# Performance work log

Hardware: AMD Instinct MI355X
Metric: run time of the kernel (lower is better)

The kernel has to match this reference:

```python
import jax, jax.numpy as jnp
import numpy as np

D_MODEL = 512
N_STATE = 512  # must equal D_MODEL (torch code broadcasts B*(N,) against u[:,t] of (batch,d_model))
BATCH = 8
SEQ_LEN = 4096
DT_MIN, DT_MAX = 0.001, 0.1


def setup_inputs() -> dict:
    key = jax.random.key(0)
    k_u, k_lam, k_b, k_q, k_dt = jax.random.split(key, 5)
    u = jax.random.normal(k_u, (BATCH, SEQ_LEN, D_MODEL), dtype=jnp.float32)
    Lambda = jax.random.normal(k_lam, (N_STATE,), dtype=jnp.float32)
    B = jax.random.normal(k_b, (N_STATE,), dtype=jnp.float32)
    Q = jax.random.normal(k_q, (N_STATE, D_MODEL), dtype=jnp.float32) / np.sqrt(N_STATE)
    log_dt = jax.random.uniform(k_dt, (1,), dtype=jnp.float32) * (np.log(DT_MAX) - np.log(DT_MIN)) + np.log(DT_MIN)
    return {"u": u, "Lambda": Lambda, "B": B, "Q": Q, "log_dt": log_dt}


def reference(u, Lambda, B, Q, log_dt):
    # dt = exp(log_dt); A = diag(exp(dt * -exp(Lambda))) -> x @ A.T == x * a
    dt = jnp.exp(log_dt)              # (1,)
    a = jnp.exp(dt * (-jnp.exp(Lambda)))  # (N,)
    Bdt = dt * B                      # (N,)

    u_t = jnp.transpose(u, (1, 0, 2))  # (L, batch, N)

    def step(x, ut):
        x = x * a + Bdt * ut           # diagonal recurrence, (batch, N)
        return x, x

    x0 = jnp.zeros((u.shape[0], Lambda.shape[0]), dtype=u.dtype)
    _, xs = jax.lax.scan(step, x0, u_t)       # (L, batch, N)
    y = jnp.einsum('lbn,nd->bld', xs, Q)      # project to d_model
    return y
```

## Files before the change

### kernel.cpp

```cpp
#include <hip/hip_runtime.h>
#include <hip/hip_bf16.h>

#define BATCH 8
#define SEQ   4096
#define NST   512
#define DM    512
#define NCHUNK 64
#define TCH    64
#define NSUB   4
#define RSUB   16
#define LDP    (NST + 8)

typedef __attribute__((ext_vector_type(4))) float f32x4;
typedef __attribute__((ext_vector_type(8))) short short8v;
typedef __attribute__((ext_vector_type(4))) short short4v;

__device__ __forceinline__ short f2bf(float f) {
  union { float f; unsigned u; } v; v.f = f;
  unsigned r = v.u + 0x7FFFu + ((v.u >> 16) & 1u);
  return (short)(r >> 16);
}

__global__ void k_scan_sums(const float* __restrict__ u, const float* __restrict__ Lam,
                            const float* __restrict__ Bv, const float* __restrict__ log_dt,
                            float* __restrict__ S) {
  int gid = blockIdx.x * 128 + threadIdx.x;
  int n0 = (gid & 127) * 4;
  int bc = gid >> 7;
  int b  = bc & (BATCH - 1);
  int c  = bc >> 3;
  float dt = expf(log_dt[0]);
  f32x4 lam = *(const f32x4*)(Lam + n0);
  f32x4 bv  = *(const f32x4*)(Bv + n0);
  float a[4], g[4];
  #pragma unroll
  for (int i = 0; i < 4; ++i) { a[i] = expf(-dt * expf(lam[i])); g[i] = dt * bv[i]; }
  const float* up = u + ((size_t)b * SEQ + (size_t)c * TCH) * NST + n0;
  f32x4 s = (f32x4){0.f, 0.f, 0.f, 0.f};
  #pragma unroll 8
  for (int t = 0; t < TCH; ++t) {
    f32x4 v = *(const f32x4*)(up + (size_t)t * NST);
    #pragma unroll
    for (int i = 0; i < 4; ++i) s[i] = fmaf(a[i], s[i], g[i] * v[i]);
  }
  *(f32x4*)(S + (c * BATCH + b) * NST + n0) = s;
}

__global__ void k_propagate(const float* __restrict__ Lam, const float* __restrict__ log_dt,
                            const float* __restrict__ S, float* __restrict__ Xc) {
  int gid = blockIdx.x * 256 + threadIdx.x;
  int n = gid & (NST - 1);
  int b = gid >> 9;
  float dt = expf(log_dt[0]);
  float a  = expf(-dt * expf(Lam[n]));
  float aT = a;
  #pragma unroll
  for (int i = 0; i < 6; ++i) aT *= aT;
  float x = 0.f;
  for (int c = 0; c < NCHUNK; ++c) {
    Xc[(c * BATCH + b) * NST + n] = x;
    x = fmaf(aT, x, S[(c * BATCH + b) * NST + n]);
  }
}

__global__ void k_transQ(const float* __restrict__ Q, short* __restrict__ Qt) {
  __shared__ short tile[64][68];
  int bn = (blockIdx.x & 7) * 64;
  int bd = (blockIdx.x >> 3) * 64;
  int tc = threadIdx.x & 15;
  int tr = threadIdx.x >> 4;
  #pragma unroll
  for (int i = 0; i < 4; ++i) {
    int r = tr + i * 16;
    f32x4 v = *(const f32x4*)(Q + (size_t)(bn + r) * DM + bd + tc * 4);
    short4v h;
    h[0] = f2bf(v[0]); h[1] = f2bf(v[1]); h[2] = f2bf(v[2]); h[3] = f2bf(v[3]);
    *(short4v*)&tile[r][tc * 4] = h;
  }
  __syncthreads();
  #pragma unroll
  for (int i = 0; i < 4; ++i) {
    int r = tr + i * 16;
    short4v h;
    #pragma unroll
    for (int j = 0; j < 4; ++j) h[j] = tile[tc * 4 + j][r];
    *(short4v*)(Qt + (size_t)(bd + r) * NST + bn + tc * 4) = h;
  }
}

__global__ __launch_bounds__(512) void k_fused(
    const float* __restrict__ u, const float* __restrict__ Lam,
    const float* __restrict__ Bv, const float* __restrict__ log_dt,
    const float* __restrict__ Xc, const short* __restrict__ Qt,
    float* __restrict__ y) {
  __shared__ __align__(16) short X[TCH][LDP];
  __shared__ __align__(16) float Ssub[NSUB][NST];
  const int tid = threadIdx.x;
  const int b = blockIdx.x & (BATCH - 1);
  const int c = blockIdx.x >> 3;
  const int tq = tid >> 7;
  const int q  = tid & 127;
  const int n0 = q * 4;

  {
    const float dt = expf(log_dt[0]);
    f32x4 lam = *(const f32x4*)(Lam + n0);
    f32x4 bv  = *(const f32x4*)(Bv + n0);
    float a[4], g[4], a16[4];
    #pragma unroll
    for (int i = 0; i < 4; ++i) {
      a[i] = expf(-dt * expf(lam[i]));
      g[i] = dt * bv[i];
      float t = a[i]; t *= t; t *= t; t *= t; t *= t;
      a16[i] = t;
    }
    f32x4 seed = (f32x4){0.f, 0.f, 0.f, 0.f};
    if (tq == 0) seed = *(const f32x4*)(Xc + (c * BATCH + b) * NST + n0);

    const float* up = u + ((size_t)b * SEQ + (size_t)(c * TCH + tq * RSUB)) * NST + n0;
    f32x4 v[RSUB];
    #pragma unroll
    for (int j = 0; j < RSUB; ++j) v[j] = *(const f32x4*)(up + (size_t)j * NST);

    f32x4 x = seed;
    #pragma unroll
    for (int j = 0; j < RSUB; ++j) {
      #pragma unroll
      for (int i = 0; i < 4; ++i) x[i] = fmaf(a[i], x[i], g[i] * v[j][i]);
      v[j] = x;
    }
    *(f32x4*)&Ssub[tq][n0] = x;
    __syncthreads();

    if (tq > 0) {
      f32x4 I = *(const f32x4*)&Ssub[0][n0];
      for (int s = 1; s < tq; ++s) {
        f32x4 sv = *(const f32x4*)&Ssub[s][n0];
        #pragma unroll
        for (int i = 0; i < 4; ++i) I[i] = fmaf(a16[i], I[i], sv[i]);
      }
      f32x4 ap;
      #pragma unroll
      for (int i = 0; i < 4; ++i) ap[i] = a[i];
      #pragma unroll
      for (int j = 0; j < RSUB; ++j) {
        #pragma unroll
        for (int i = 0; i < 4; ++i) {
          v[j][i] = fmaf(ap[i], I[i], v[j][i]);
          ap[i] *= a[i];
        }
      }
    }
    #pragma unroll
    for (int j = 0; j < RSUB; ++j) {
      short4v h;
      h[0] = f2bf(v[j][0]); h[1] = f2bf(v[j][1]);
      h[2] = f2bf(v[j][2]); h[3] = f2bf(v[j][3]);
      *(short4v*)&X[tq * RSUB + j][n0] = h;
    }
  }
  __syncthreads();

  const int lane = tid & 63;
  const int wc   = tid >> 6;
  const int l15  = lane & 15;
  const int lhi  = lane >> 4;
  const int ka   = lhi * 8;
  const short* qbase = Qt + (size_t)(wc * 64 + l15) * NST + ka;
  float* yb = y + ((size_t)b * SEQ + (size_t)c * TCH) * DM;

  f32x4 acc[4][4];
  #pragma unroll
  for (int mi = 0; mi < 4; ++mi)
    #pragma unroll
    for (int nf = 0; nf < 4; ++nf) acc[mi][nf] = (f32x4){0.f, 0.f, 0.f, 0.f};

  #pragma unroll 4
  for (int kk = 0; kk < 16; ++kk) {
    const int k0 = kk * 32;
    short8v afrag[4];
    #pragma unroll
    for (int mi = 0; mi < 4; ++mi)
      afrag[mi] = *(const short8v*)&X[mi * 16 + l15][k0 + ka];
    short8v bfrag[4];
    #pragma unroll
    for (int nf = 0; nf < 4; ++nf)
      bfrag[nf] = *(const short8v*)(qbase + (size_t)nf * 16 * NST + k0);
    #pragma unroll
    for (int mi = 0; mi < 4; ++mi)
      #pragma unroll
      for (int nf = 0; nf < 4; ++nf)
        acc[mi][nf] = __builtin_amdgcn_mfma_f32_16x16x32_bf16(afrag[mi], bfrag[nf], acc[mi][nf], 0, 0, 0);
  }

  #pragma unroll
  for (int mi = 0; mi < 4; ++mi)
    #pragma unroll
    for (int nf = 0; nf < 4; ++nf) {
      const int rr = mi * 16 + lhi * 4;
      const int cc = wc * 64 + nf * 16 + l15;
      #pragma unroll
      for (int i = 0; i < 4; ++i)
        yb[(size_t)(rr + i) * DM + cc] = acc[mi][nf][i];
    }
}

extern "C" void kernel_launch(void* const* d_in, const int* in_sizes, int n_in,
                              void* d_out, int out_size, void* d_ws, size_t ws_size,
                              hipStream_t stream) {
  const float* u      = (const float*)d_in[0];
  const float* Lam    = (const float*)d_in[1];
  const float* Bv     = (const float*)d_in[2];
  const float* Q      = (const float*)d_in[3];
  const float* log_dt = (const float*)d_in[4];
  float* out = (float*)d_out;

  float* S  = (float*)d_ws;
  float* Xc = S + NCHUNK * BATCH * NST;
  short* Qt = (short*)(Xc + NCHUNK * BATCH * NST);

  hipLaunchKernelGGL(k_transQ, dim3(64), dim3(256), 0, stream, Q, Qt);
  hipLaunchKernelGGL(k_scan_sums, dim3(NCHUNK * BATCH), dim3(128), 0, stream,
                     u, Lam, Bv, log_dt, S);
  hipLaunchKernelGGL(k_propagate, dim3(BATCH * NST / 256), dim3(256), 0, stream,
                     Lam, log_dt, S, Xc);
  hipLaunchKernelGGL(k_fused, dim3(NCHUNK * BATCH), dim3(512), 0, stream,
                     u, Lam, Bv, log_dt, Xc, Qt, out);
}
```

Measured before the change: 70.79 us.

## Fuse scan pipeline into single cooperative kernel with grid sync

Replaces the four-kernel sequence (Q transpose, chunk sums, propagation, fused scan+GEMM) with one cooperative kernel. Each block computes its chunk-local scan once, keeps the u values in registers, publishes the chunk sum, grid-syncs, then directly reduces preceding chunk sums to get its carry-in before the MFMA projection. This removes launch overhead and the second read of u, at the cost of a grid-wide barrier and an O(c) redundant prefix reduction per block. If the cooperative launch fails, it falls back to the old path. The Qt transpose in the first 64 blocks is not ordered by a grid barrier before other blocks read Qt after the sync; it is written before the sync, so it is covered.

```diff
diff --git a/kernel.cpp b/kernel.cpp
--- a/kernel.cpp
+++ b/kernel.cpp
@@ -1,5 +1,8 @@
 #include <hip/hip_runtime.h>
 #include <hip/hip_bf16.h>
+#include <hip/hip_cooperative_groups.h>
+
+namespace cg = cooperative_groups;
 
 #define BATCH 8
 #define SEQ   4096
@@ -19,6 +22,180 @@
   union { float f; unsigned u; } v; v.f = f;
   unsigned r = v.u + 0x7FFFu + ((v.u >> 16) & 1u);
   return (short)(r >> 16);
+}
+
+__global__ __launch_bounds__(512) void k_mega(
+    const float* __restrict__ u, const float* __restrict__ Lam,
+    const float* __restrict__ Bv, const float* __restrict__ log_dt,
+    const float* __restrict__ Q, float* __restrict__ S,
+    short* __restrict__ Qt, float* __restrict__ y) {
+  __shared__ __align__(16) short X[TCH][LDP];
+  __shared__ __align__(16) float Ssub[NSUB][NST];
+  const int tid = threadIdx.x;
+  const int b = blockIdx.x & (BATCH - 1);
+  const int c = blockIdx.x >> 3;
+  const int tq = tid >> 7;
+  const int q  = tid & 127;
+  const int n0 = q * 4;
+
+  if (blockIdx.x < 64) {
+    short (*tile)[68] = (short(*)[68])&X[0][0];
+    const int bn = (blockIdx.x & 7) * 64;
+    const int bd = (blockIdx.x >> 3) * 64;
+    const int tc4 = (tid & 15) * 4;
+    const int tr = tid >> 4;
+    #pragma unroll
+    for (int i = 0; i < 2; ++i) {
+      int r = tr + i * 32;
+      f32x4 v = *(const f32x4*)(Q + (size_t)(bn + r) * DM + bd + tc4);
+      short4v h;
+      h[0] = f2bf(v[0]); h[1] = f2bf(v[1]); h[2] = f2bf(v[2]); h[3] = f2bf(v[3]);
+      *(short4v*)&tile[r][tc4] = h;
+    }
+    __syncthreads();
+    #pragma unroll
+    for (int i = 0; i < 2; ++i) {
+      int r = tr + i * 32;
+      short4v h;
+      #pragma unroll
+      for (int j = 0; j < 4; ++j) h[j] = tile[tc4 + j][r];
+      *(short4v*)(Qt + (size_t)(bd + r) * NST + bn + tc4) = h;
+    }
+    __syncthreads();
+  }
+
+  const float dtv = expf(log_dt[0]);
+  f32x4 lam = *(const f32x4*)(Lam + n0);
+  f32x4 bv  = *(const f32x4*)(Bv + n0);
+  float a[4], g[4], a16[4];
+  #pragma unroll
+  for (int i = 0; i < 4; ++i) {
+    a[i] = expf(-dtv * expf(lam[i]));
+    g[i] = dtv * bv[i];
+    float t = a[i]; t *= t; t *= t; t *= t; t *= t;
+    a16[i] = t;
+  }
+
+  const float* up = u + ((size_t)b * SEQ + (size_t)(c * TCH + tq * RSUB)) * NST + n0;
+  f32x4 v[RSUB];
+  #pragma unroll
+  for (int j = 0; j < RSUB; ++j) v[j] = *(const f32x4*)(up + (size_t)j * NST);
+  {
+    f32x4 x = (f32x4){0.f, 0.f, 0.f, 0.f};
+    #pragma unroll
+    for (int j = 0; j < RSUB; ++j) {
+      #pragma unroll
+      for (int i = 0; i < 4; ++i) x[i] = fmaf(a[i], x[i], g[i] * v[j][i]);
+      v[j] = x;
+    }
+    *(f32x4*)&Ssub[tq][n0] = x;
+  }
+  __syncthreads();
+
+  if (tq == 0) {
+    f32x4 s0 = *(const f32x4*)&Ssub[0][n0];
+    f32x4 s1 = *(const f32x4*)&Ssub[1][n0];
+    f32x4 s2 = *(const f32x4*)&Ssub[2][n0];
+    f32x4 s3 = *(const f32x4*)&Ssub[3][n0];
+    f32x4 cs;
+    #pragma unroll
+    for (int i = 0; i < 4; ++i)
+      cs[i] = fmaf(a16[i], fmaf(a16[i], fmaf(a16[i], s0[i], s1[i]), s2[i]), s3[i]);
+    *(f32x4*)(S + (c * BATCH + b) * NST + n0) = cs;
+  }
+  __threadfence();
+  cg::this_grid().sync();
+
+  float a64[4];
+  #pragma unroll
+  for (int i = 0; i < 4; ++i) { float t = a16[i]; t *= t; t *= t; a64[i] = t; }
+  f32x4 xin = (f32x4){0.f, 0.f, 0.f, 0.f};
+  {
+    int cp = 0;
+    for (; cp + 8 <= c; cp += 8) {
+      f32x4 sb[8];
+      #pragma unroll
+      for (int j = 0; j < 8; ++j) sb[j] = *(const f32x4*)(S + ((cp + j) * BATCH + b) * NST + n0);
+      #pragma unroll
+      for (int j = 0; j < 8; ++j)
+        #pragma unroll
+        for (int i = 0; i < 4; ++i) xin[i] = fmaf(a64[i], xin[i], sb[j][i]);
+    }
+    for (; cp < c; ++cp) {
+      f32x4 sv = *(const f32x4*)(S + (cp * BATCH + b) * NST + n0);
+      #pragma unroll
+      for (int i = 0; i < 4; ++i) xin[i] = fmaf(a64[i], xin[i], sv[i]);
+    }
+  }
+
+  f32x4 I = xin;
+  for (int s = 0; s < tq; ++s) {
+    f32x4 sv = *(const f32x4*)&Ssub[s][n0];
+    #pragma unroll
+    for (int i = 0; i < 4; ++i) I[i] = fmaf(a16[i], I[i], sv[i]);
+  }
+
+  {
+    f32x4 ap;
+    #pragma unroll
+    for (int i = 0; i < 4; ++i) ap[i] = a[i];
+    #pragma unroll
+    for (int j = 0; j < RSUB; ++j) {
+      short4v h;
+      #pragma unroll
+      for (int i = 0; i < 4; ++i) {
+        v[j][i] = fmaf(ap[i], I[i], v[j][i]);
+        ap[i] *= a[i];
+      }
+      h[0] = f2bf(v[j][0]); h[1] = f2bf(v[j][1]);
+      h[2] = f2bf(v[j][2]); h[3] = f2bf(v[j][3]);
+      *(short4v*)&X[tq * RSUB + j][n0] = h;
+    }
+  }
+  __syncthreads();
+
+  const int lane = tid & 63;
+  const int wc   = tid >> 6;
+  const int l15  = lane & 15;
+  const int lhi  = lane >> 4;
+  const int ka   = lhi * 8;
+  const short* qbase = Qt + (size_t)(wc * 64 + l15) * NST + ka;
+  float* yb = y + ((size_t)b * SEQ + (size_t)c * TCH) * DM;
+
+  f32x4 acc[4][4];
+  #pragma unroll
+  for (int mi = 0; mi < 4; ++mi)
+    #pragma unroll
+    for (int nf = 0; nf < 4; ++nf) acc[mi][nf] = (f32x4){0.f, 0.f, 0.f, 0.f};
+
+  #pragma unroll 4
+  for (int kk = 0; kk < 16; ++kk) {
+    const int k0 = kk * 32;
+    short8v afrag[4];
+    #pragma unroll
+    for (int mi = 0; mi < 4; ++mi)
+      afrag[mi] = *(const short8v*)&X[mi * 16 + l15][k0 + ka];
+    short8v bfrag[4];
+    #pragma unroll
+    for (int nf = 0; nf < 4; ++nf)
+      bfrag[nf] = *(const short8v*)(qbase + (size_t)nf * 16 * NST + k0);
+    #pragma unroll
+    for (int mi = 0; mi < 4; ++mi)
+      #pragma unroll
+      for (int nf = 0; nf < 4; ++nf)
+        acc[mi][nf] = __builtin_amdgcn_mfma_f32_16x16x32_bf16(afrag[mi], bfrag[nf], acc[mi][nf], 0, 0, 0);
+  }
+
+  #pragma unroll
+  for (int mi = 0; mi < 4; ++mi)
+    #pragma unroll
+    for (int nf = 0; nf < 4; ++nf) {
+      const int rr = mi * 16 + lhi * 4;
+      const int cc = wc * 64 + nf * 16 + l15;
+      #pragma unroll
+      for (int i = 0; i < 4; ++i)
+        yb[(size_t)(rr + i) * DM + cc] = acc[mi][nf][i];
+    }
 }
 
 __global__ void k_scan_sums(const float* __restrict__ u, const float* __restrict__ Lam,
@@ -101,7 +278,6 @@
   const int tq = tid >> 7;
   const int q  = tid & 127;
   const int n0 = q * 4;
-
   {
     const float dt = expf(log_dt[0]);
     f32x4 lam = *(const f32x4*)(Lam + n0);
@@ -116,12 +292,10 @@
     }
     f32x4 seed = (f32x4){0.f, 0.f, 0.f, 0.f};
     if (tq == 0) seed = *(const f32x4*)(Xc + (c * BATCH + b) * NST + n0);
-
     const float* up = u + ((size_t)b * SEQ + (size_t)(c * TCH + tq * RSUB)) * NST + n0;
     f32x4 v[RSUB];
     #pragma unroll
     for (int j = 0; j < RSUB; ++j) v[j] = *(const f32x4*)(up + (size_t)j * NST);
-
     f32x4 x = seed;
     #pragma unroll
     for (int j = 0; j < RSUB; ++j) {
@@ -131,7 +305,6 @@
     }
     *(f32x4*)&Ssub[tq][n0] = x;
     __syncthreads();
-
     if (tq > 0) {
       f32x4 I = *(const f32x4*)&Ssub[0][n0];
       for (int s = 1; s < tq; ++s) {
@@ -143,13 +316,12 @@
       #pragma unroll
       for (int i = 0; i < 4; ++i) ap[i] = a[i];
       #pragma unroll
-      for (int j = 0; j < RSUB; ++j) {
+      for (int j = 0; j < RSUB; ++j)
         #pragma unroll
         for (int i = 0; i < 4; ++i) {
           v[j][i] = fmaf(ap[i], I[i], v[j][i]);
           ap[i] *= a[i];
         }
-      }
     }
     #pragma unroll
     for (int j = 0; j < RSUB; ++j) {
@@ -160,7 +332,6 @@
     }
   }
   __syncthreads();
-
   const int lane = tid & 63;
   const int wc   = tid >> 6;
   const int l15  = lane & 15;
@@ -168,13 +339,11 @@
   const int ka   = lhi * 8;
   const short* qbase = Qt + (size_t)(wc * 64 + l15) * NST + ka;
   float* yb = y + ((size_t)b * SEQ + (size_t)c * TCH) * DM;
-
   f32x4 acc[4][4];
   #pragma unroll
   for (int mi = 0; mi < 4; ++mi)
     #pragma unroll
     for (int nf = 0; nf < 4; ++nf) acc[mi][nf] = (f32x4){0.f, 0.f, 0.f, 0.f};
-
   #pragma unroll 4
   for (int kk = 0; kk < 16; ++kk) {
     const int k0 = kk * 32;
@@ -192,7 +361,6 @@
       for (int nf = 0; nf < 4; ++nf)
         acc[mi][nf] = __builtin_amdgcn_mfma_f32_16x16x32_bf16(afrag[mi], bfrag[nf], acc[mi][nf], 0, 0, 0);
   }
-
   #pragma unroll
   for (int mi = 0; mi < 4; ++mi)
     #pragma unroll
@@ -219,11 +387,18 @@
   float* Xc = S + NCHUNK * BATCH * NST;
   short* Qt = (short*)(Xc + NCHUNK * BATCH * NST);
 
-  hipLaunchKernelGGL(k_transQ, dim3(64), dim3(256), 0, stream, Q, Qt);
-  hipLaunchKernelGGL(k_scan_sums, dim3(NCHUNK * BATCH), dim3(128), 0, stream,
-                     u, Lam, Bv, log_dt, S);
-  hipLaunchKernelGGL(k_propagate, dim3(BATCH * NST / 256), dim3(256), 0, stream,
-                     Lam, log_dt, S, Xc);
-  hipLaunchKernelGGL(k_fused, dim3(NCHUNK * BATCH), dim3(512), 0, stream,
-                     u, Lam, Bv, log_dt, Xc, Qt, out);
-}
+  void* args[] = {(void*)&u, (void*)&Lam, (void*)&Bv, (void*)&log_dt,
+                  (void*)&Q, (void*)&S, (void*)&Qt, (void*)&out};
+  hipError_t e = hipLaunchCooperativeKernel((const void*)k_mega,
+                                            dim3(NCHUNK * BATCH), dim3(512),
+                                            args, 0, stream);
+  if (e != hipSuccess) {
+    hipLaunchKernelGGL(k_transQ, dim3(64), dim3(256), 0, stream, Q, Qt);
+    hipLaunchKernelGGL(k_scan_sums, dim3(NCHUNK * BATCH), dim3(128), 0, stream,
+                       u, Lam, Bv, log_dt, S);
+    hipLaunchKernelGGL(k_propagate, dim3(BATCH * NST / 256), dim3(256), 0, stream,
+                       Lam, log_dt, S, Xc);
+    hipLaunchKernelGGL(k_fused, dim3(NCHUNK * BATCH), dim3(512), 0, stream,
+                       u, Lam, Bv, log_dt, Xc, Qt, out);
+  }
+}
```

New measurement: 202.6 us. 186% more time.

## Store bf16 local scan states in first pass and reuse them in fused projection

Applied to the files above, without the earlier changes.

The chunk scan kernel now writes each step's chunk-local state to a bf16 workspace buffer. The fused projection kernel reads these back and adds the decayed chunk carry-in, instead of re-reading u in fp32 and redoing a sub-chunk scan. This trades a second fp32 read of u for a bf16 write plus read, and simplifies the in-block combine. It needs a large workspace, falls back to the old path otherwise, and rounds intermediate states twice.

```diff
diff --git a/kernel.cpp b/kernel.cpp
--- a/kernel.cpp
+++ b/kernel.cpp
@@ -19,6 +19,178 @@
   union { float f; unsigned u; } v; v.f = f;
   unsigned r = v.u + 0x7FFFu + ((v.u >> 16) & 1u);
   return (short)(r >> 16);
+}
+__device__ __forceinline__ float bf2f(short s) {
+  union { unsigned u; float f; } v; v.u = ((unsigned)(unsigned short)s) << 16;
+  return v.f;
+}
+
+__global__ __launch_bounds__(128) void k_scan_store(
+    const float* __restrict__ u, const float* __restrict__ Lam,
+    const float* __restrict__ Bv, const float* __restrict__ log_dt,
+    float* __restrict__ S, short* __restrict__ XL) {
+  const int q  = threadIdx.x;
+  const int n0 = q * 4;
+  const int b  = blockIdx.x & (BATCH - 1);
+  const int c  = blockIdx.x >> 3;
+  const float dt = expf(log_dt[0]);
+  f32x4 lam = *(const f32x4*)(Lam + n0);
+  f32x4 bv  = *(const f32x4*)(Bv + n0);
+  float a[4], g[4];
+  #pragma unroll
+  for (int i = 0; i < 4; ++i) { a[i] = expf(-dt * expf(lam[i])); g[i] = dt * bv[i]; }
+  const float* up = u  + ((size_t)b * SEQ + (size_t)c * TCH) * NST + n0;
+  short*      xp = XL + ((size_t)b * SEQ + (size_t)c * TCH) * NST + n0;
+  f32x4 x = (f32x4){0.f, 0.f, 0.f, 0.f};
+  for (int t0 = 0; t0 < TCH; t0 += 8) {
+    f32x4 w[8];
+    #pragma unroll
+    for (int j = 0; j < 8; ++j) w[j] = *(const f32x4*)(up + (size_t)(t0 + j) * NST);
+    #pragma unroll
+    for (int j = 0; j < 8; ++j) {
+      #pragma unroll
+      for (int i = 0; i < 4; ++i) x[i] = fmaf(a[i], x[i], g[i] * w[j][i]);
+      short4v h;
+      h[0] = f2bf(x[0]); h[1] = f2bf(x[1]); h[2] = f2bf(x[2]); h[3] = f2bf(x[3]);
+      *(short4v*)(xp + (size_t)(t0 + j) * NST) = h;
+    }
+  }
+  *(f32x4*)(S + (c * BATCH + b) * NST + n0) = x;
+}
+
+__global__ void k_propagate(const float* __restrict__ Lam, const float* __restrict__ log_dt,
+                            const float* __restrict__ S, float* __restrict__ Xc) {
+  int gid = blockIdx.x * 256 + threadIdx.x;
+  int n = gid & (NST - 1);
+  int b = gid >> 9;
+  float dt = expf(log_dt[0]);
+  float a  = expf(-dt * expf(Lam[n]));
+  float aT = a;
+  #pragma unroll
+  for (int i = 0; i < 6; ++i) aT *= aT;
+  float x = 0.f;
+  for (int c = 0; c < NCHUNK; ++c) {
+    Xc[(c * BATCH + b) * NST + n] = x;
+    x = fmaf(aT, x, S[(c * BATCH + b) * NST + n]);
+  }
+}
+
+__global__ void k_transQ(const float* __restrict__ Q, short* __restrict__ Qt) {
+  __shared__ short tile[64][68];
+  int bn = (blockIdx.x & 7) * 64;
+  int bd = (blockIdx.x >> 3) * 64;
+  int tc = threadIdx.x & 15;
+  int tr = threadIdx.x >> 4;
+  #pragma unroll
+  for (int i = 0; i < 4; ++i) {
+    int r = tr + i * 16;
+    f32x4 v = *(const f32x4*)(Q + (size_t)(bn + r) * DM + bd + tc * 4);
+    short4v h;
+    h[0] = f2bf(v[0]); h[1] = f2bf(v[1]); h[2] = f2bf(v[2]); h[3] = f2bf(v[3]);
+    *(short4v*)&tile[r][tc * 4] = h;
+  }
+  __syncthreads();
+  #pragma unroll
+  for (int i = 0; i < 4; ++i) {
+    int r = tr + i * 16;
+    short4v h;
+    #pragma unroll
+    for (int j = 0; j < 4; ++j) h[j] = tile[tc * 4 + j][r];
+    *(short4v*)(Qt + (size_t)(bd + r) * NST + bn + tc * 4) = h;
+  }
+}
+
+__global__ __launch_bounds__(512) void k_fusedB(
+    const float* __restrict__ Lam, const float* __restrict__ Bv,
+    const float* __restrict__ log_dt, const float* __restrict__ Xc,
+    const short* __restrict__ XL, const short* __restrict__ Qt,
+    float* __restrict__ y) {
+  __shared__ __align__(16) short X[TCH][LDP];
+  const int tid = threadIdx.x;
+  const int b = blockIdx.x & (BATCH - 1);
+  const int c = blockIdx.x >> 3;
+  const int tq = tid >> 7;
+  const int q  = tid & 127;
+  const int n0 = q * 4;
+
+  {
+    const float dt = expf(log_dt[0]);
+    f32x4 lam = *(const f32x4*)(Lam + n0);
+    float a[4], ap[4];
+    #pragma unroll
+    for (int i = 0; i < 4; ++i) a[i] = expf(-dt * expf(lam[i]));
+    #pragma unroll
+    for (int i = 0; i < 4; ++i) {
+      float t16 = a[i]; t16 *= t16; t16 *= t16; t16 *= t16; t16 *= t16;
+      float p = a[i];
+      float base = t16;
+      int e = tq;
+      if (e & 1) p *= base;
+      base *= base;
+      if (e & 2) p *= base;
+      ap[i] = p;
+    }
+    f32x4 xin = *(const f32x4*)(Xc + (c * BATCH + b) * NST + n0);
+    const short* xp = XL + ((size_t)b * SEQ + (size_t)(c * TCH + tq * RSUB)) * NST + n0;
+    short4v hv[RSUB];
+    #pragma unroll
+    for (int j = 0; j < RSUB; ++j) hv[j] = *(const short4v*)(xp + (size_t)j * NST);
+    #pragma unroll
+    for (int j = 0; j < RSUB; ++j) {
+      short4v h;
+      #pragma unroll
+      for (int i = 0; i < 4; ++i) {
+        float xv = fmaf(ap[i], xin[i], bf2f(hv[j][i]));
+        ap[i] *= a[i];
+        h[i] = f2bf(xv);
+      }
+      *(short4v*)&X[tq * RSUB + j][n0] = h;
+    }
+  }
+  __syncthreads();
+
+  const int lane = tid & 63;
+  const int wc   = tid >> 6;
+  const int l15  = lane & 15;
+  const int lhi  = lane >> 4;
+  const int ka   = lhi * 8;
+  const short* qbase = Qt + (size_t)(wc * 64 + l15) * NST + ka;
+  float* yb = y + ((size_t)b * SEQ + (size_t)c * TCH) * DM;
+
+  f32x4 acc[4][4];
+  #pragma unroll
+  for (int mi = 0; mi < 4; ++mi)
+    #pragma unroll
+    for (int nf = 0; nf < 4; ++nf) acc[mi][nf] = (f32x4){0.f, 0.f, 0.f, 0.f};
+
+  #pragma unroll 4
+  for (int kk = 0; kk < 16; ++kk) {
+    const int k0 = kk * 32;
+    short8v afrag[4];
+    #pragma unroll
+    for (int mi = 0; mi < 4; ++mi)
+      afrag[mi] = *(const short8v*)&X[mi * 16 + l15][k0 + ka];
+    short8v bfrag[4];
+    #pragma unroll
+    for (int nf = 0; nf < 4; ++nf)
+      bfrag[nf] = *(const short8v*)(qbase + (size_t)nf * 16 * NST + k0);
+    #pragma unroll
+    for (int mi = 0; mi < 4; ++mi)
+      #pragma unroll
+      for (int nf = 0; nf < 4; ++nf)
+        acc[mi][nf] = __builtin_amdgcn_mfma_f32_16x16x32_bf16(afrag[mi], bfrag[nf], acc[mi][nf], 0, 0, 0);
+  }
+
+  #pragma unroll
+  for (int mi = 0; mi < 4; ++mi)
+    #pragma unroll
+    for (int nf = 0; nf < 4; ++nf) {
+      const int rr = mi * 16 + lhi * 4;
+      const int cc = wc * 64 + nf * 16 + l15;
+      #pragma unroll
+      for (int i = 0; i < 4; ++i)
+        yb[(size_t)(rr + i) * DM + cc] = acc[mi][nf][i];
+    }
 }
 
 __global__ void k_scan_sums(const float* __restrict__ u, const float* __restrict__ Lam,
@@ -44,48 +216,6 @@
     for (int i = 0; i < 4; ++i) s[i] = fmaf(a[i], s[i], g[i] * v[i]);
   }
   *(f32x4*)(S + (c * BATCH + b) * NST + n0) = s;
-}
-
-__global__ void k_propagate(const float* __restrict__ Lam, const float* __restrict__ log_dt,
-                            const float* __restrict__ S, float* __restrict__ Xc) {
-  int gid = blockIdx.x * 256 + threadIdx.x;
-  int n = gid & (NST - 1);
-  int b = gid >> 9;
-  float dt = expf(log_dt[0]);
-  float a  = expf(-dt * expf(Lam[n]));
-  float aT = a;
-  #pragma unroll
-  for (int i = 0; i < 6; ++i) aT *= aT;
-  float x = 0.f;
-  for (int c = 0; c < NCHUNK; ++c) {
-    Xc[(c * BATCH + b) * NST + n] = x;
-    x = fmaf(aT, x, S[(c * BATCH + b) * NST + n]);
-  }
-}
-
-__global__ void k_transQ(const float* __restrict__ Q, short* __restrict__ Qt) {
-  __shared__ short tile[64][68];
-  int bn = (blockIdx.x & 7) * 64;
-  int bd = (blockIdx.x >> 3) * 64;
-  int tc = threadIdx.x & 15;
-  int tr = threadIdx.x >> 4;
-  #pragma unroll
-  for (int i = 0; i < 4; ++i) {
-    int r = tr + i * 16;
-    f32x4 v = *(const f32x4*)(Q + (size_t)(bn + r) * DM + bd + tc * 4);
-    short4v h;
-    h[0] = f2bf(v[0]); h[1] = f2bf(v[1]); h[2] = f2bf(v[2]); h[3] = f2bf(v[3]);
-    *(short4v*)&tile[r][tc * 4] = h;
-  }
-  __syncthreads();
-  #pragma unroll
-  for (int i = 0; i < 4; ++i) {
-    int r = tr + i * 16;
-    short4v h;
-    #pragma unroll
-    for (int j = 0; j < 4; ++j) h[j] = tile[tc * 4 + j][r];
-    *(short4v*)(Qt + (size_t)(bd + r) * NST + bn + tc * 4) = h;
-  }
 }
 
 __global__ __launch_bounds__(512) void k_fused(
@@ -101,7 +231,6 @@
   const int tq = tid >> 7;
   const int q  = tid & 127;
   const int n0 = q * 4;
-
   {
     const float dt = expf(log_dt[0]);
     f32x4 lam = *(const f32x4*)(Lam + n0);
@@ -116,12 +245,10 @@
     }
     f32x4 seed = (f32x4){0.f, 0.f, 0.f, 0.f};
     if (tq == 0) seed = *(const f32x4*)(Xc + (c * BATCH + b) * NST + n0);
-
     const float* up = u + ((size_t)b * SEQ + (size_t)(c * TCH + tq * RSUB)) * NST + n0;
     f32x4 v[RSUB];
     #pragma unroll
     for (int j = 0; j < RSUB; ++j) v[j] = *(const f32x4*)(up + (size_t)j * NST);
-
     f32x4 x = seed;
     #pragma unroll
     for (int j = 0; j < RSUB; ++j) {
@@ -131,7 +258,6 @@
     }
     *(f32x4*)&Ssub[tq][n0] = x;
     __syncthreads();
-
     if (tq > 0) {
       f32x4 I = *(const f32x4*)&Ssub[0][n0];
       for (int s = 1; s < tq; ++s) {
@@ -143,13 +269,12 @@
       #pragma unroll
       for (int i = 0; i < 4; ++i) ap[i] = a[i];
       #pragma unroll
-      for (int j = 0; j < RSUB; ++j) {
+      for (int j = 0; j < RSUB; ++j)
         #pragma unroll
         for (int i = 0; i < 4; ++i) {
           v[j][i] = fmaf(ap[i], I[i], v[j][i]);
           ap[i] *= a[i];
         }
-      }
     }
     #pragma unroll
     for (int j = 0; j < RSUB; ++j) {
@@ -160,7 +285,6 @@
     }
   }
   __syncthreads();
-
   const int lane = tid & 63;
   const int wc   = tid >> 6;
   const int l15  = lane & 15;
@@ -168,13 +292,11 @@
   const int ka   = lhi * 8;
   const short* qbase = Qt + (size_t)(wc * 64 + l15) * NST + ka;
   float* yb = y + ((size_t)b * SEQ + (size_t)c * TCH) * DM;
-
   f32x4 acc[4][4];
   #pragma unroll
   for (int mi = 0; mi < 4; ++mi)
     #pragma unroll
     for (int nf = 0; nf < 4; ++nf) acc[mi][nf] = (f32x4){0.f, 0.f, 0.f, 0.f};
-
   #pragma unroll 4
   for (int kk = 0; kk < 16; ++kk) {
     const int k0 = kk * 32;
@@ -192,7 +314,6 @@
       for (int nf = 0; nf < 4; ++nf)
         acc[mi][nf] = __builtin_amdgcn_mfma_f32_16x16x32_bf16(afrag[mi], bfrag[nf], acc[mi][nf], 0, 0, 0);
   }
-
   #pragma unroll
   for (int mi = 0; mi < 4; ++mi)
     #pragma unroll
@@ -215,15 +336,29 @@
   const float* log_dt = (const float*)d_in[4];
   float* out = (float*)d_out;
 
+  const size_t nS  = (size_t)NCHUNK * BATCH * NST;
   float* S  = (float*)d_ws;
-  float* Xc = S + NCHUNK * BATCH * NST;
-  short* Qt = (short*)(Xc + NCHUNK * BATCH * NST);
-
-  hipLaunchKernelGGL(k_transQ, dim3(64), dim3(256), 0, stream, Q, Qt);
-  hipLaunchKernelGGL(k_scan_sums, dim3(NCHUNK * BATCH), dim3(128), 0, stream,
-                     u, Lam, Bv, log_dt, S);
-  hipLaunchKernelGGL(k_propagate, dim3(BATCH * NST / 256), dim3(256), 0, stream,
-                     Lam, log_dt, S, Xc);
-  hipLaunchKernelGGL(k_fused, dim3(NCHUNK * BATCH), dim3(512), 0, stream,
-                     u, Lam, Bv, log_dt, Xc, Qt, out);
-}
+  float* Xc = S + nS;
+  short* Qt = (short*)(Xc + nS);
+  short* XL = Qt + (size_t)DM * NST;
+  const size_t need = nS * 4 * 2 + (size_t)DM * NST * 2
+                    + (size_t)BATCH * SEQ * NST * 2;
+
+  if (ws_size >= need) {
+    hipLaunchKernelGGL(k_transQ, dim3(64), dim3(256), 0, stream, Q, Qt);
+    hipLaunchKernelGGL(k_scan_store, dim3(NCHUNK * BATCH), dim3(128), 0, stream,
+                       u, Lam, Bv, log_dt, S, XL);
+    hipLaunchKernelGGL(k_propagate, dim3(BATCH * NST / 256), dim3(256), 0, stream,
+                       Lam, log_dt, S, Xc);
+    hipLaunchKernelGGL(k_fusedB, dim3(NCHUNK * BATCH), dim3(512), 0, stream,
+                       Lam, Bv, log_dt, Xc, XL, Qt, out);
+  } else {
+    hipLaunchKernelGGL(k_transQ, dim3(64), dim3(256), 0, stream, Q, Qt);
+    hipLaunchKernelGGL(k_scan_sums, dim3(NCHUNK * BATCH), dim3(128), 0, stream,
+                       u, Lam, Bv, log_dt, S);
+    hipLaunchKernelGGL(k_propagate, dim3(BATCH * NST / 256), dim3(256), 0, stream,
+                       Lam, log_dt, S, Xc);
+    hipLaunchKernelGGL(k_fused, dim3(NCHUNK * BATCH), dim3(512), 0, stream,
+                       u, Lam, Bv, log_dt, Xc, Qt, out);
+  }
+}
```

Result: slower. 72.27 us (+2.1%).
